# Kernel optimization log

Hardware: AMD Instinct MI355X
Metric: run time of the kernel (lower is better)

The kernel has to match this reference:

```python
import jax, jax.numpy as jnp
import numpy as np

R = 64
N = 7

_D_PARMS = [[1], [0, 1], [8, 1, 1], [16, 25, 3, 1], [260, 153, 65, 6, 1],
            [1856, 21, 629, 137, 10, 1], [26240, 26603, 11253, 1990, 263, 15, 1]]

def _get_variance(n, r):
    res = 0.0
    for i, x in enumerate(_D_PARMS[n - 1]):
        x = float(x)
        for j in range(i):
            x *= (r - j)
        res += x
    return res

_DECAYS = [1.0] + [float(np.sqrt(_get_variance(i + 1, R) / _get_variance(i, R)))
                   for i in range(1, N)]
_DECAY_CUMSUM = float(np.sqrt(N))


def setup_inputs() -> dict:
    key = jax.random.key(0)
    M = jax.random.normal(key, (8192, R * R), dtype=jnp.float32)
    return {"M": M}


def reference(M) -> jnp.ndarray:
    shape = M.shape[:-1]
    Mm = M.reshape(shape + (R, R))            # [..., r, r]
    # power series: cumsum = sum_i (M^(i+1)) / prod(decays[:i+1]) (decays[0]=1)
    P = Mm
    acc = Mm
    for i in range(1, N):                     # fixed N=7 unrolled chain
        P = jnp.matmul(P, Mm) / _DECAYS[i]
        acc = acc + P
    # NOTE: the torch code's cumsum[..., mask, mask].zero_() operates on a copy
    # (advanced indexing), so it is a no-op on cumsum; we faithfully omit it.
    acc = acc / _DECAY_CUMSUM
    return acc.reshape(shape + (R * R,))
```

## Files before the change

### kernel.cpp

```cpp
#include <hip/hip_runtime.h>
#include <hip/hip_bf16.h>
#include <math.h>


#define RDIM 64
#define MSTR 68

using bf16x8 = __attribute__((ext_vector_type(8))) short;
using f32x4  = __attribute__((ext_vector_type(4))) float;

static __device__ __forceinline__ short f2bf(float x) {
    union { __hip_bfloat16 b; short s; } u; u.b = __float2bfloat16(x); return u.s;
}
static __device__ __forceinline__ float bf2f(short s) {
    union { short s2[2]; float f; } u; u.s2[0] = 0; u.s2[1] = s; return u.f;
}

__global__ __launch_bounds__(256, 3) void power_series_kernel(
        const float* __restrict__ M, float* __restrict__ out) {
    __shared__ float Ms[RDIM][MSTR];

    const int tid  = threadIdx.x;
    const int w    = tid >> 6;
    const int lane = tid & 63;
    const int q    = lane >> 4;
    const int l    = lane & 15;

    const float* Mg = M   + (size_t)blockIdx.x * (RDIM * RDIM);
    float*       Og = out + (size_t)blockIdx.x * (RDIM * RDIM);

    {
        const float4* Mg4 = reinterpret_cast<const float4*>(Mg);
        #pragma unroll
        for (int v = 0; v < 4; ++v) {
            int e = tid + 256 * v;
            float4 x = Mg4[e];
            int row = (e * 4) >> 6, col = (e * 4) & 63;
            *reinterpret_cast<float4*>(&Ms[row][col]) = x;
        }
    }
    __syncthreads();

    bf16x8 amhi[4][2], amlo[4][2];
    #pragma unroll
    for (int t = 0; t < 4; ++t) {
        #pragma unroll
        for (int kb = 0; kb < 2; ++kb) {
            const float* src = &Ms[16 * t + l][32 * kb + 8 * q];
            float4 x0 = *reinterpret_cast<const float4*>(src);
            float4 x1 = *reinterpret_cast<const float4*>(src + 4);
            float xs[8] = {x0.x, x0.y, x0.z, x0.w, x1.x, x1.y, x1.z, x1.w};
            bf16x8 hv, lv;
            #pragma unroll
            for (int j = 0; j < 8; ++j) {
                short h = f2bf(xs[j]); hv[j] = h;
                lv[j] = f2bf(xs[j] - bf2f(h));
            }
            amhi[t][kb] = hv; amlo[t][kb] = lv;
        }
    }

    bf16x8 pbhi[2], pblo[2];
    #pragma unroll
    for (int kb = 0; kb < 2; ++kb) {
        float xs[8];
        #pragma unroll
        for (int jj = 0; jj < 8; ++jj) {
            int j = (jj + 2 * q) & 7;
            xs[j] = Ms[32 * kb + 8 * q + j][16 * w + l];
        }
        bf16x8 hv, lv;
        #pragma unroll
        for (int j = 0; j < 8; ++j) {
            short h = f2bf(xs[j]); hv[j] = h;
            lv[j] = f2bf(xs[j] - bf2f(h));
        }
        pbhi[kb] = hv; pblo[kb] = lv;
    }

    const int sA    = 2 * (q & 1) + (q >> 1);
    const int addrA = ((sA << 4) + l) << 2;
    const int addrB = ((((sA ^ 1)) << 4) + l) << 2;
    const int qlo   = q & 1;
    const int qhi   = q >> 1;

    const double V[7] = {1.0, 64.0, 4104.0, 263696.0, 17021060.0,
                         1104218816.0, 72260728960.0};
    float invd[7];
    invd[0] = 1.0f;
    #pragma unroll
    for (int i = 1; i < 7; ++i) invd[i] = (float)(1.0 / sqrt(V[i] / V[i - 1]));

    f32x4 acc[4];
    #pragma unroll
    for (int t = 0; t < 4; ++t) acc[t] = (f32x4){0.f, 0.f, 0.f, 0.f};

    #pragma unroll
    for (int s = 1; s <= 6; ++s) {
        f32x4 c[4];
        #pragma unroll
        for (int t = 0; t < 4; ++t) {
            f32x4 cc = (f32x4){0.f, 0.f, 0.f, 0.f};
            cc = __builtin_amdgcn_mfma_f32_16x16x32_bf16(amhi[t][0], pbhi[0], cc, 0, 0, 0);
            cc = __builtin_amdgcn_mfma_f32_16x16x32_bf16(amhi[t][1], pbhi[1], cc, 0, 0, 0);
            cc = __builtin_amdgcn_mfma_f32_16x16x32_bf16(amhi[t][0], pblo[0], cc, 0, 0, 0);
            cc = __builtin_amdgcn_mfma_f32_16x16x32_bf16(amhi[t][1], pblo[1], cc, 0, 0, 0);
            cc = __builtin_amdgcn_mfma_f32_16x16x32_bf16(amlo[t][0], pbhi[0], cc, 0, 0, 0);
            cc = __builtin_amdgcn_mfma_f32_16x16x32_bf16(amlo[t][1], pbhi[1], cc, 0, 0, 0);
            c[t] = cc;
        }
        const float inv = invd[s];

        if (s < 6) {
            int pdh[4][2], pdl[4][2];
            #pragma unroll
            for (int t = 0; t < 4; ++t) {
                #pragma unroll
                for (int h = 0; h < 2; ++h) {
                    float a0 = c[t][2 * h] * inv, a1 = c[t][2 * h + 1] * inv;
                    acc[t][2 * h] += a0; acc[t][2 * h + 1] += a1;
                    short h0 = f2bf(a0), h1 = f2bf(a1);
                    pdh[t][h] = (h0 & 0xffff) | ((int)h1 << 16);
                    short g0 = f2bf(a0 - bf2f(h0)), g1 = f2bf(a1 - bf2f(h1));
                    pdl[t][h] = (g0 & 0xffff) | ((int)g1 << 16);
                }
            }
            union { int d[4]; bf16x8 v; } nh[2], nl[2];
            #pragma unroll
            for (int kb = 0; kb < 2; ++kb) {
                #pragma unroll
                for (int h = 0; h < 2; ++h) {
                    int zA = qlo ? pdh[2 * kb + 1][h] : pdh[2 * kb][h];
                    int zB = qlo ? pdh[2 * kb][h]     : pdh[2 * kb + 1][h];
                    int rA = __builtin_amdgcn_ds_bpermute(addrA, zA);
                    int rB = __builtin_amdgcn_ds_bpermute(addrB, zB);
                    nh[kb].d[h]     = qhi ? rB : rA;
                    nh[kb].d[2 + h] = qhi ? rA : rB;
                    zA = qlo ? pdl[2 * kb + 1][h] : pdl[2 * kb][h];
                    zB = qlo ? pdl[2 * kb][h]     : pdl[2 * kb + 1][h];
                    rA = __builtin_amdgcn_ds_bpermute(addrA, zA);
                    rB = __builtin_amdgcn_ds_bpermute(addrB, zB);
                    nl[kb].d[h]     = qhi ? rB : rA;
                    nl[kb].d[2 + h] = qhi ? rA : rB;
                }
            }
            pbhi[0] = nh[0].v; pbhi[1] = nh[1].v;
            pblo[0] = nl[0].v; pblo[1] = nl[1].v;
        } else {
            #pragma unroll
            for (int t = 0; t < 4; ++t)
                #pragma unroll
                for (int r = 0; r < 4; ++r)
                    acc[t][r] += c[t][r] * inv;
        }
    }

    const float oscale = 0.3779644730092272f;
    #pragma unroll
    for (int t = 0; t < 4; ++t) {
        #pragma unroll
        for (int r = 0; r < 4; ++r) {
            int row = 16 * t + 4 * q + r;
            int col = 16 * w + l;
            Og[row * 64 + col] = (acc[t][r] + Ms[row][col]) * oscale;
        }
    }
}

extern "C" void kernel_launch(void* const* d_in, const int* in_sizes, int n_in,
                              void* d_out, int out_size, void* d_ws, size_t ws_size,
                              hipStream_t stream) {
    const float* M = (const float*)d_in[0];
    float* out = (float*)d_out;
    const int nmat = in_sizes[0] / (RDIM * RDIM);
    power_series_kernel<<<dim3(nmat), dim3(256), 0, stream>>>(M, out);
}
```

Before: 283.1 us.

## Truncate-split via byte perm, interleave MFMA with permutes, coalesce output stores

Replaces the bf16 round-to-nearest conversion with truncation-based hi/lo splitting using v_perm, which cuts ALU work in the split loops. Each step's MFMAs are interleaved per k-block with the conversion and bpermute work so that work can overlap. The decay constants move to a host-computed kernel argument, and launch bounds are raised to request 4 blocks per CU. Output is staged through shared memory so it can be written with coalesced float4 stores instead of strided scalar stores, at the cost of two extra barriers.

```diff
diff --git a/kernel.cpp b/kernel.cpp
--- a/kernel.cpp
+++ b/kernel.cpp
@@ -9,15 +9,26 @@
 using bf16x8 = __attribute__((ext_vector_type(8))) short;
 using f32x4  = __attribute__((ext_vector_type(4))) float;
 
-static __device__ __forceinline__ short f2bf(float x) {
-    union { __hip_bfloat16 b; short s; } u; u.b = __float2bfloat16(x); return u.s;
+union FU { float f; unsigned u; };
+static __device__ __forceinline__ unsigned fbits(float x) { FU v; v.f = x; return v.u; }
+static __device__ __forceinline__ float ubits(unsigned x) { FU v; v.u = x; return v.f; }
+
+static __device__ __forceinline__ void split2(float a0, float a1,
+                                              unsigned& hd, unsigned& ld) {
+    const unsigned SEL = 0x07060302u;
+    unsigned u0 = fbits(a0), u1 = fbits(a1);
+    hd = __builtin_amdgcn_perm(u1, u0, SEL);
+    float r0 = a0 - ubits(u0 & 0xffff0000u);
+    float r1 = a1 - ubits(u1 & 0xffff0000u);
+    ld = __builtin_amdgcn_perm(fbits(r1), fbits(r0), SEL);
 }
-static __device__ __forceinline__ float bf2f(short s) {
-    union { short s2[2]; float f; } u; u.s2[0] = 0; u.s2[1] = s; return u.f;
-}
-
-__global__ __launch_bounds__(256, 3) void power_series_kernel(
-        const float* __restrict__ M, float* __restrict__ out) {
+
+struct Decays { float inv[8]; };
+
+#define MFMA(a, b, c) __builtin_amdgcn_mfma_f32_16x16x32_bf16(a, b, c, 0, 0, 0)
+
+__global__ __launch_bounds__(256, 4) void power_series_kernel(
+        const float* __restrict__ M, float* __restrict__ out, Decays dec) {
     __shared__ float Ms[RDIM][MSTR];
 
     const int tid  = threadIdx.x;
@@ -41,6 +52,8 @@
     }
     __syncthreads();
 
+    union V8 { unsigned d[4]; bf16x8 v; };
+
     bf16x8 amhi[4][2], amlo[4][2];
     #pragma unroll
     for (int t = 0; t < 4; ++t) {
@@ -50,13 +63,11 @@
             float4 x0 = *reinterpret_cast<const float4*>(src);
             float4 x1 = *reinterpret_cast<const float4*>(src + 4);
             float xs[8] = {x0.x, x0.y, x0.z, x0.w, x1.x, x1.y, x1.z, x1.w};
-            bf16x8 hv, lv;
+            V8 hv, lv;
             #pragma unroll
-            for (int j = 0; j < 8; ++j) {
-                short h = f2bf(xs[j]); hv[j] = h;
-                lv[j] = f2bf(xs[j] - bf2f(h));
-            }
-            amhi[t][kb] = hv; amlo[t][kb] = lv;
+            for (int dd = 0; dd < 4; ++dd)
+                split2(xs[2 * dd], xs[2 * dd + 1], hv.d[dd], lv.d[dd]);
+            amhi[t][kb] = hv.v; amlo[t][kb] = lv.v;
         }
     }
 
@@ -69,13 +80,11 @@
             int j = (jj + 2 * q) & 7;
             xs[j] = Ms[32 * kb + 8 * q + j][16 * w + l];
         }
-        bf16x8 hv, lv;
-        #pragma unroll
-        for (int j = 0; j < 8; ++j) {
-            short h = f2bf(xs[j]); hv[j] = h;
-            lv[j] = f2bf(xs[j] - bf2f(h));
-        }
-        pbhi[kb] = hv; pblo[kb] = lv;
+        V8 hv, lv;
+        #pragma unroll
+        for (int dd = 0; dd < 4; ++dd)
+            split2(xs[2 * dd], xs[2 * dd + 1], hv.d[dd], lv.d[dd]);
+        pbhi[kb] = hv.v; pblo[kb] = lv.v;
     }
 
     const int sA    = 2 * (q & 1) + (q >> 1);
@@ -84,66 +93,59 @@
     const int qlo   = q & 1;
     const int qhi   = q >> 1;
 
-    const double V[7] = {1.0, 64.0, 4104.0, 263696.0, 17021060.0,
-                         1104218816.0, 72260728960.0};
-    float invd[7];
-    invd[0] = 1.0f;
-    #pragma unroll
-    for (int i = 1; i < 7; ++i) invd[i] = (float)(1.0 / sqrt(V[i] / V[i - 1]));
-
     f32x4 acc[4];
     #pragma unroll
     for (int t = 0; t < 4; ++t) acc[t] = (f32x4){0.f, 0.f, 0.f, 0.f};
 
     #pragma unroll
     for (int s = 1; s <= 6; ++s) {
+        const float inv = dec.inv[s];
         f32x4 c[4];
-        #pragma unroll
-        for (int t = 0; t < 4; ++t) {
-            f32x4 cc = (f32x4){0.f, 0.f, 0.f, 0.f};
-            cc = __builtin_amdgcn_mfma_f32_16x16x32_bf16(amhi[t][0], pbhi[0], cc, 0, 0, 0);
-            cc = __builtin_amdgcn_mfma_f32_16x16x32_bf16(amhi[t][1], pbhi[1], cc, 0, 0, 0);
-            cc = __builtin_amdgcn_mfma_f32_16x16x32_bf16(amhi[t][0], pblo[0], cc, 0, 0, 0);
-            cc = __builtin_amdgcn_mfma_f32_16x16x32_bf16(amhi[t][1], pblo[1], cc, 0, 0, 0);
-            cc = __builtin_amdgcn_mfma_f32_16x16x32_bf16(amlo[t][0], pbhi[0], cc, 0, 0, 0);
-            cc = __builtin_amdgcn_mfma_f32_16x16x32_bf16(amlo[t][1], pbhi[1], cc, 0, 0, 0);
-            c[t] = cc;
-        }
-        const float inv = invd[s];
-
-        if (s < 6) {
-            int pdh[4][2], pdl[4][2];
+        unsigned pdh[4][2], pdl[4][2];
+        V8 nh[2], nl[2];
+        #pragma unroll
+        for (int kb = 0; kb < 2; ++kb) {
             #pragma unroll
-            for (int t = 0; t < 4; ++t) {
+            for (int tt = 0; tt < 2; ++tt) {
+                int t = 2 * kb + tt;
+                f32x4 cc = (f32x4){0.f, 0.f, 0.f, 0.f};
+                cc = MFMA(amhi[t][0], pbhi[0], cc);
+                cc = MFMA(amhi[t][1], pbhi[1], cc);
+                cc = MFMA(amhi[t][0], pblo[0], cc);
+                cc = MFMA(amhi[t][1], pblo[1], cc);
+                cc = MFMA(amlo[t][0], pbhi[0], cc);
+                cc = MFMA(amlo[t][1], pbhi[1], cc);
+                c[t] = cc;
+            }
+            if (s < 6) {
+                #pragma unroll
+                for (int tt = 0; tt < 2; ++tt) {
+                    int t = 2 * kb + tt;
+                    #pragma unroll
+                    for (int h = 0; h < 2; ++h) {
+                        float a0 = c[t][2 * h] * inv, a1 = c[t][2 * h + 1] * inv;
+                        acc[t][2 * h] += a0; acc[t][2 * h + 1] += a1;
+                        split2(a0, a1, pdh[t][h], pdl[t][h]);
+                    }
+                }
                 #pragma unroll
                 for (int h = 0; h < 2; ++h) {
-                    float a0 = c[t][2 * h] * inv, a1 = c[t][2 * h + 1] * inv;
-                    acc[t][2 * h] += a0; acc[t][2 * h + 1] += a1;
-                    short h0 = f2bf(a0), h1 = f2bf(a1);
-                    pdh[t][h] = (h0 & 0xffff) | ((int)h1 << 16);
-                    short g0 = f2bf(a0 - bf2f(h0)), g1 = f2bf(a1 - bf2f(h1));
-                    pdl[t][h] = (g0 & 0xffff) | ((int)g1 << 16);
-                }
-            }
-            union { int d[4]; bf16x8 v; } nh[2], nl[2];
-            #pragma unroll
-            for (int kb = 0; kb < 2; ++kb) {
-                #pragma unroll
-                for (int h = 0; h < 2; ++h) {
-                    int zA = qlo ? pdh[2 * kb + 1][h] : pdh[2 * kb][h];
-                    int zB = qlo ? pdh[2 * kb][h]     : pdh[2 * kb + 1][h];
+                    int zA = qlo ? (int)pdh[2 * kb + 1][h] : (int)pdh[2 * kb][h];
+                    int zB = qlo ? (int)pdh[2 * kb][h]     : (int)pdh[2 * kb + 1][h];
                     int rA = __builtin_amdgcn_ds_bpermute(addrA, zA);
                     int rB = __builtin_amdgcn_ds_bpermute(addrB, zB);
                     nh[kb].d[h]     = qhi ? rB : rA;
                     nh[kb].d[2 + h] = qhi ? rA : rB;
-                    zA = qlo ? pdl[2 * kb + 1][h] : pdl[2 * kb][h];
-                    zB = qlo ? pdl[2 * kb][h]     : pdl[2 * kb + 1][h];
+                    zA = qlo ? (int)pdl[2 * kb + 1][h] : (int)pdl[2 * kb][h];
+                    zB = qlo ? (int)pdl[2 * kb][h]     : (int)pdl[2 * kb + 1][h];
                     rA = __builtin_amdgcn_ds_bpermute(addrA, zA);
                     rB = __builtin_amdgcn_ds_bpermute(addrB, zB);
                     nl[kb].d[h]     = qhi ? rB : rA;
                     nl[kb].d[2 + h] = qhi ? rA : rB;
                 }
             }
+        }
+        if (s < 6) {
             pbhi[0] = nh[0].v; pbhi[1] = nh[1].v;
             pblo[0] = nl[0].v; pblo[1] = nl[1].v;
         } else {
@@ -156,13 +158,26 @@
     }
 
     const float oscale = 0.3779644730092272f;
-    #pragma unroll
-    for (int t = 0; t < 4; ++t) {
-        #pragma unroll
-        for (int r = 0; r < 4; ++r) {
-            int row = 16 * t + 4 * q + r;
-            int col = 16 * w + l;
-            Og[row * 64 + col] = (acc[t][r] + Ms[row][col]) * oscale;
+    float o[4][4];
+    #pragma unroll
+    for (int t = 0; t < 4; ++t)
+        #pragma unroll
+        for (int r = 0; r < 4; ++r)
+            o[t][r] = (acc[t][r] + Ms[16 * t + 4 * q + r][16 * w + l]) * oscale;
+    __syncthreads();
+    #pragma unroll
+    for (int t = 0; t < 4; ++t)
+        #pragma unroll
+        for (int r = 0; r < 4; ++r)
+            Ms[16 * t + 4 * q + r][16 * w + l] = o[t][r];
+    __syncthreads();
+    {
+        float4* Og4 = reinterpret_cast<float4*>(Og);
+        #pragma unroll
+        for (int v = 0; v < 4; ++v) {
+            int e = tid + 256 * v;
+            int row = (e * 4) >> 6, col = (e * 4) & 63;
+            Og4[e] = *reinterpret_cast<const float4*>(&Ms[row][col]);
         }
     }
 }
@@ -173,5 +188,13 @@
     const float* M = (const float*)d_in[0];
     float* out = (float*)d_out;
     const int nmat = in_sizes[0] / (RDIM * RDIM);
-    power_series_kernel<<<dim3(nmat), dim3(256), 0, stream>>>(M, out);
+
+    static const double V[7] = {1.0, 64.0, 4104.0, 263696.0, 17021060.0,
+                                1104218816.0, 72260728960.0};
+    Decays dec;
+    dec.inv[0] = 1.0f;
+    for (int i = 1; i < 7; ++i) dec.inv[i] = (float)(1.0 / sqrt(V[i] / V[i - 1]));
+    dec.inv[7] = 0.0f;
+
+    power_series_kernel<<<dim3(nmat), dim3(256), 0, stream>>>(M, out, dec);
 }
```

New measurement: 496.5 us. +75.4%, slower.
